# Kernel tuning notes

Measured on AMD Instinct MI355X. Metric: run time of the kernel, lower is better.

## Reference

```python
import jax, jax.numpy as jnp
import numpy as np

B, T, D, H = 4, 2048, 1024, 16
Dh = D // H          # 64 head dim
NF = Dh // 2         # 32 rotary frequencies


def setup_inputs() -> dict:
    key = jax.random.key(0)
    k0, k1, k2, k3 = jax.random.split(key, 4)
    x = jax.random.normal(k0, (B, T, D), dtype=jnp.float32)
    # 3D spatial coordinates per token, e.g. voxel positions
    coords = jax.random.uniform(k1, (B, T, 3), dtype=jnp.float32, minval=0.0, maxval=64.0)
    w_scale = 1.0 / np.sqrt(D)
    qkv_w = jax.random.normal(k2, (3 * D, D), dtype=jnp.float32) * w_scale
    qkv_b = jnp.zeros((3 * D,), dtype=jnp.float32)
    proj_w = jax.random.normal(k3, (D, D), dtype=jnp.float32) * w_scale
    proj_b = jnp.zeros((D,), dtype=jnp.float32)
    # mixed-axis rope: frequency f uses coordinate axis (f % 3), geometric period spacing within each axis group
    axes = (jnp.arange(NF) % 3).astype(jnp.int32)
    group = (jnp.arange(NF) // 3).astype(jnp.float32)
    n_per_axis = float(NF) / 3.0
    inv_freq = (10000.0 ** (-group / n_per_axis)).astype(jnp.float32)
    return {"x": x, "coords": coords, "qkv_w": qkv_w, "qkv_b": qkv_b,
            "proj_w": proj_w, "proj_b": proj_b, "inv_freq": inv_freq, "axes": axes}


def _apply_rope(t, sin, cos):
    # t: [B, H, T, Dh]; sin/cos: [B, 1, T, Dh//2]  (rotate-half convention)
    t1, t2 = jnp.split(t, 2, axis=-1)
    return jnp.concatenate([t1 * cos - t2 * sin, t1 * sin + t2 * cos], axis=-1)


def reference(x, coords, qkv_w, qkv_b, proj_w, proj_b, inv_freq, axes):
    b, t, d = x.shape
    # fused QKV projection
    qkv = (x @ qkv_w.T + qkv_b).reshape(b, t, 3, H, Dh)
    qkv = jnp.transpose(qkv, (2, 0, 3, 1, 4))     # [3, B, H, T, Dh]
    q, k, v = qkv[0], qkv[1], qkv[2]
    # vectorized per-sample rope from coords (replaces python loop over batch)
    ang = jnp.take(coords, axes, axis=-1) * inv_freq      # [B, T, NF]
    sin = jnp.sin(ang)[:, None]                            # [B, 1, T, NF]
    cos = jnp.cos(ang)[:, None]
    q = _apply_rope(q, sin, cos)
    k = _apply_rope(k, sin, cos)
    # standard scaling mode: single 1/sqrt(Dh) inside SDPA
    scale = 1.0 / np.sqrt(Dh)
    scores = jnp.einsum('bhqd,bhkd->bhqk', q, k) * scale
    attn = jax.nn.softmax(scores, axis=-1)
    out = jnp.einsum('bhqk,bhkd->bhqd', attn, v)           # [B, H, T, Dh]
    out = jnp.transpose(out, (0, 2, 1, 3)).reshape(b, t, d)
    return out @ proj_w.T + proj_b
```

## Files before the change

kernel.cpp:

```cpp
#include <hip/hip_runtime.h>
#include <hip/hip_bf16.h>

#define B_ 4
#define T_ 2048
#define D_ 1024
#define H_ 16
#define DH 64
#define NF 32
#define BH (B_*H_)
#define M_ROWS (B_*T_)

using u16 = unsigned short;
using u32 = unsigned int;

typedef __bf16 bf16x8 __attribute__((ext_vector_type(8)));
typedef float  f32x4  __attribute__((ext_vector_type(4)));

__device__ __forceinline__ u16 f2bf(float f) {
  u32 u = __float_as_uint(f);
  u32 r = u + 0x7fffu + ((u >> 16) & 1u);
  return (u16)(r >> 16);
}
__device__ __forceinline__ u16 f2bf_hw(float f) {
  __bf16 h = (__bf16)f;
  return *(u16*)&h;
}
__device__ __forceinline__ float bf2f(u16 h) {
  return __uint_as_float(((u32)h) << 16);
}

__device__ __forceinline__ void gload_lds16(const void* g, void* l) {
  __builtin_amdgcn_global_load_lds((__attribute__((address_space(1))) void*)(g),
                                   (__attribute__((address_space(3))) void*)(l),
                                   16, 0, 0);
}

__global__ __launch_bounds__(256)
void cvt_kernel(const float* __restrict__ in, u16* __restrict__ out, int n8) {
  int idx = blockIdx.x * 256 + threadIdx.x;
  if (idx >= n8) return;
  const float4* p = (const float4*)in + (long)idx * 2;
  float4 a = p[0], b = p[1];
  u32 o0 = (u32)f2bf(a.x) | ((u32)f2bf(a.y) << 16);
  u32 o1 = (u32)f2bf(a.z) | ((u32)f2bf(a.w) << 16);
  u32 o2 = (u32)f2bf(b.x) | ((u32)f2bf(b.y) << 16);
  u32 o3 = (u32)f2bf(b.z) | ((u32)f2bf(b.w) << 16);
  ((uint4*)out)[idx] = make_uint4(o0, o1, o2, o3);
}

__global__ __launch_bounds__(256)
void sincos_kernel(const float* __restrict__ coords, const float* __restrict__ inv_freq,
                   const int* __restrict__ axes, float* __restrict__ sc) {
  int idx = blockIdx.x * 256 + threadIdx.x;
  if (idx >= B_ * T_ * NF) return;
  int f = idx & 31;
  long bt = idx >> 5;
  float c = coords[bt * 3 + axes[f]];
  float ang = c * inv_freq[f];
  sc[bt * 64 + f]      = sinf(ang);
  sc[bt * 64 + 32 + f] = cosf(ang);
}

template<int OUT_F32>
__global__ __launch_bounds__(256, 2)
void gemm_bt(const u16* __restrict__ A, const u16* __restrict__ Bt,
             const float* __restrict__ bias, void* __restrict__ Cout,
             int M, int N, int K) {
  __shared__ u16 As[128 * 64];
  __shared__ u16 Bs[128 * 64];
  int nb = N >> 7;
  int bid = blockIdx.x;
  int nwg = gridDim.x;
  if ((nwg & 7) == 0) {
    int c = nwg >> 3;
    bid = (bid & 7) * c + (bid >> 3);
  }
  int bm = bid / nb, bn = bid % nb;
  long m0 = (long)bm << 7, n0 = (long)bn << 7;
  int tid = threadIdx.x;
  int lane = tid & 63, w = tid >> 6;
  int g = lane >> 4, lr = lane & 15;
  int wm = w >> 1, wn = w & 1;

  f32x4 acc[4][4] = {};

  for (int kt = 0; kt < K; kt += 64) {
    __syncthreads();
    #pragma unroll
    for (int j = 0; j < 4; ++j) {
      int ob = j * 4096 + tid * 16;
      int row = ob >> 7, col = (ob & 127) >> 1;
      u16* ldsA = As + j * 2048 + w * 512;
      u16* ldsB = Bs + j * 2048 + w * 512;
      gload_lds16(A + (m0 + row) * K + kt + col, ldsA);
      gload_lds16(Bt + (n0 + row) * K + kt + col, ldsB);
    }
    __syncthreads();
    #pragma unroll
    for (int kk = 0; kk < 2; ++kk) {
      bf16x8 af[4], bfr[4];
      #pragma unroll
      for (int i = 0; i < 4; ++i)
        af[i] = *(const bf16x8*)(As + (wm * 64 + i * 16 + lr) * 64 + kk * 32 + g * 8);
      #pragma unroll
      for (int i = 0; i < 4; ++i)
        bfr[i] = *(const bf16x8*)(Bs + (wn * 64 + i * 16 + lr) * 64 + kk * 32 + g * 8);
      #pragma unroll
      for (int mi = 0; mi < 4; ++mi)
        #pragma unroll
        for (int nj = 0; nj < 4; ++nj)
          acc[mi][nj] = __builtin_amdgcn_mfma_f32_16x16x32_bf16(af[mi], bfr[nj], acc[mi][nj], 0, 0, 0);
    }
  }
  #pragma unroll
  for (int mi = 0; mi < 4; ++mi) {
    #pragma unroll
    for (int nj = 0; nj < 4; ++nj) {
      long col = n0 + wn * 64 + nj * 16 + lr;
      float bv = bias[col];
      #pragma unroll
      for (int i = 0; i < 4; ++i) {
        long row = m0 + wm * 64 + mi * 16 + g * 4 + i;
        float v = acc[mi][nj][i] + bv;
        if (OUT_F32) ((float*)Cout)[row * (long)N + col] = v;
        else         ((u16*)Cout)[row * (long)N + col] = f2bf(v);
      }
    }
  }
}

__global__ __launch_bounds__(256)
void rope_kernel(const u16* __restrict__ qkv, const float* __restrict__ sc,
                 u16* __restrict__ qr, u16* __restrict__ kr, u16* __restrict__ vt) {
  __shared__ u16 Vsm[128 * 72];
  int bh = blockIdx.y;
  int b = bh >> 4, h = bh & 15;
  int t0 = blockIdx.x << 7;
  int tid = threadIdx.x;

  #pragma unroll
  for (int part = 0; part < 2; ++part) {
    u16* outp = part ? kr : qr;
    float qscale = part ? 1.0f : 0.125f;
    #pragma unroll
    for (int it = 0; it < 2; ++it) {
      int item = it * 256 + tid;
      int tl = item >> 2, fg = item & 3;
      long t = t0 + tl;
      long rbase = ((long)(b * T_) + t) * 3072 + part * 1024 + h * 64 + fg * 8;
      uint4 u1 = *(const uint4*)(qkv + rbase);
      uint4 u2 = *(const uint4*)(qkv + rbase + 32);
      const float* scp = sc + ((long)(b * T_) + t) * 64 + fg * 8;
      float4 sn0 = *(const float4*)(scp);
      float4 sn1 = *(const float4*)(scp + 4);
      float4 cs0 = *(const float4*)(scp + 32);
      float4 cs1 = *(const float4*)(scp + 36);
      float sn[8], cs[8], f1[8], f2[8];
      u32 w1[4] = {u1.x, u1.y, u1.z, u1.w};
      u32 w2[4] = {u2.x, u2.y, u2.z, u2.w};
      #pragma unroll
      for (int j = 0; j < 4; ++j) {
        f1[2*j]   = bf2f((u16)(w1[j] & 0xffff));
        f1[2*j+1] = bf2f((u16)(w1[j] >> 16));
        f2[2*j]   = bf2f((u16)(w2[j] & 0xffff));
        f2[2*j+1] = bf2f((u16)(w2[j] >> 16));
      }
      sn[0]=sn0.x; sn[1]=sn0.y; sn[2]=sn0.z; sn[3]=sn0.w;
      sn[4]=sn1.x; sn[5]=sn1.y; sn[6]=sn1.z; sn[7]=sn1.w;
      cs[0]=cs0.x; cs[1]=cs0.y; cs[2]=cs0.z; cs[3]=cs0.w;
      cs[4]=cs1.x; cs[5]=cs1.y; cs[6]=cs1.z; cs[7]=cs1.w;
      u32 o1[4], o2[4];
      #pragma unroll
      for (int j = 0; j < 4; ++j) {
        u16 a0 = f2bf((f1[2*j]   * cs[2*j]   - f2[2*j]   * sn[2*j])   * qscale);
        u16 a1 = f2bf((f1[2*j+1] * cs[2*j+1] - f2[2*j+1] * sn[2*j+1]) * qscale);
        u16 b0 = f2bf((f1[2*j]   * sn[2*j]   + f2[2*j]   * cs[2*j])   * qscale);
        u16 b1 = f2bf((f1[2*j+1] * sn[2*j+1] + f2[2*j+1] * cs[2*j+1]) * qscale);
        o1[j] = (u32)a0 | ((u32)a1 << 16);
        o2[j] = (u32)b0 | ((u32)b1 << 16);
      }
      long obase = ((long)bh * T_ + t) * DH + fg * 8;
      *(uint4*)(outp + obase)      = make_uint4(o1[0], o1[1], o1[2], o1[3]);
      *(uint4*)(outp + obase + 32) = make_uint4(o2[0], o2[1], o2[2], o2[3]);
    }
  }
  #pragma unroll
  for (int it = 0; it < 4; ++it) {
    int item = it * 256 + tid;
    int tl = item >> 3, dg = item & 7;
    long t = t0 + tl;
    uint4 u = *(const uint4*)(qkv + ((long)(b * T_) + t) * 3072 + 2048 + h * 64 + dg * 8);
    *(uint4*)(Vsm + tl * 72 + dg * 8) = u;
  }
  __syncthreads();
  int d = tid >> 2, tc = tid & 3;
  long obase = ((long)bh * DH + d) * T_ + t0 + tc * 32;
  #pragma unroll
  for (int c = 0; c < 4; ++c) {
    u32 o[4];
    #pragma unroll
    for (int j = 0; j < 4; ++j) {
      u16 lo = Vsm[(tc * 32 + c * 8 + 2 * j)     * 72 + d];
      u16 hi = Vsm[(tc * 32 + c * 8 + 2 * j + 1) * 72 + d];
      o[j] = (u32)lo | ((u32)hi << 16);
    }
    *(uint4*)(vt + obase + c * 8) = make_uint4(o[0], o[1], o[2], o[3]);
  }
}

__global__ __launch_bounds__(256, 3)
void attn_kernel(const u16* __restrict__ Qr, const u16* __restrict__ Kr,
                 const u16* __restrict__ Vt, u16* __restrict__ Aout) {
  __shared__ u16 Ks[2][64 * 64];
  __shared__ u16 Vs[2][64 * 64];
  __shared__ u16 Ps[4][32 * 72];
  int wg = (blockIdx.x & 7) * 128 + (blockIdx.x >> 3);
  int bh = wg >> 4;
  int b = bh >> 4, h = bh & 15;
  int q0 = (wg & 15) << 7;
  int tid = threadIdx.x;
  int lane = tid & 63, w = tid >> 6;
  int g = lane >> 4, lr = lane & 15;

  const long tbase = (long)bh * T_;
  const long vbase = (long)bh * DH;

  bf16x8 aq[2][2];
  #pragma unroll
  for (int mi = 0; mi < 2; ++mi)
    #pragma unroll
    for (int kk = 0; kk < 2; ++kk)
      aq[mi][kk] = *(const bf16x8*)(Qr + (tbase + q0 + w * 32 + mi * 16 + lr) * DH + kk * 32 + g * 8);

  f32x4 oacc[2][4] = {};
  float lsum[2][4] = {};

  const int swz0 = ((0 + g) ^ (lr & 7)) << 3;
  const int swz1 = ((4 + g) ^ (lr & 7)) << 3;

  auto STAGE = [&](int buf, int kb) {
    #pragma unroll
    for (int j = 0; j < 2; ++j) {
      int ob = j * 4096 + tid * 16;
      int row = ob >> 7;
      int c = ((ob >> 4) & 7) ^ (row & 7);
      u16* ldsK = Ks[buf] + j * 2048 + w * 512;
      u16* ldsV = Vs[buf] + j * 2048 + w * 512;
      gload_lds16(Kr + (tbase + kb + row) * DH + c * 8, ldsK);
      gload_lds16(Vt + (vbase + row) * T_ + kb + c * 8, ldsV);
    }
  };

  STAGE(0, 0);
  asm volatile("s_waitcnt vmcnt(0)" ::: "memory");
  __builtin_amdgcn_s_barrier();
  __builtin_amdgcn_sched_barrier(0);

  int cur = 0;
  for (int kt = 0; kt < T_ / 64; ++kt) {
    if (kt + 1 < T_ / 64) STAGE(cur ^ 1, (kt + 1) * 64);

    const u16* kbuf = Ks[cur];
    const u16* vbuf = Vs[cur];

    f32x4 s[2][4] = {};
    #pragma unroll
    for (int kk = 0; kk < 2; ++kk) {
      int so = kk ? swz1 : swz0;
      bf16x8 bk[4];
      #pragma unroll
      for (int nj = 0; nj < 4; ++nj)
        bk[nj] = *(const bf16x8*)(kbuf + (nj * 16 + lr) * 64 + so);
      #pragma unroll
      for (int mi = 0; mi < 2; ++mi)
        #pragma unroll
        for (int nj = 0; nj < 4; ++nj)
          s[mi][nj] = __builtin_amdgcn_mfma_f32_16x16x32_bf16(aq[mi][kk], bk[nj], s[mi][nj], 0, 0, 0);
    }

    u16* pw = Ps[w];
    #pragma unroll
    for (int mi = 0; mi < 2; ++mi) {
      #pragma unroll
      for (int i = 0; i < 4; ++i) {
        float p0 = __expf(s[mi][0][i]);
        float p1 = __expf(s[mi][1][i]);
        float p2 = __expf(s[mi][2][i]);
        float p3 = __expf(s[mi][3][i]);
        lsum[mi][i] += (p0 + p1) + (p2 + p3);
        int rb = (mi * 16 + g * 4 + i) * 72 + lr;
        pw[rb]      = f2bf_hw(p0);
        pw[rb + 16] = f2bf_hw(p1);
        pw[rb + 32] = f2bf_hw(p2);
        pw[rb + 48] = f2bf_hw(p3);
      }
    }
    asm volatile("s_waitcnt lgkmcnt(0)" ::: "memory");
    __builtin_amdgcn_sched_barrier(0);

    #pragma unroll
    for (int kk = 0; kk < 2; ++kk) {
      int so = kk ? swz1 : swz0;
      bf16x8 ap[2], bv[4];
      #pragma unroll
      for (int mi = 0; mi < 2; ++mi)
        ap[mi] = *(const bf16x8*)(pw + (mi * 16 + lr) * 72 + kk * 32 + g * 8);
      #pragma unroll
      for (int nj = 0; nj < 4; ++nj)
        bv[nj] = *(const bf16x8*)(vbuf + (nj * 16 + lr) * 64 + so);
      #pragma unroll
      for (int mi = 0; mi < 2; ++mi)
        #pragma unroll
        for (int nj = 0; nj < 4; ++nj)
          oacc[mi][nj] = __builtin_amdgcn_mfma_f32_16x16x32_bf16(ap[mi], bv[nj], oacc[mi][nj], 0, 0, 0);
    }

    __builtin_amdgcn_sched_barrier(0);
    asm volatile("s_waitcnt vmcnt(0)" ::: "memory");
    __builtin_amdgcn_s_barrier();
    __builtin_amdgcn_sched_barrier(0);
    cur ^= 1;
  }

  #pragma unroll
  for (int mi = 0; mi < 2; ++mi) {
    #pragma unroll
    for (int i = 0; i < 4; ++i) {
      float l = lsum[mi][i];
      #pragma unroll
      for (int dd = 1; dd < 16; dd <<= 1) l += __shfl_xor(l, dd);
      float inv = 1.0f / l;
      long q = q0 + w * 32 + mi * 16 + g * 4 + i;
      long obase = ((long)b * T_ + q) * D_ + h * DH;
      #pragma unroll
      for (int nj = 0; nj < 4; ++nj)
        Aout[obase + nj * 16 + lr] = f2bf_hw(oacc[mi][nj][i] * inv);
    }
  }
}

extern "C" void kernel_launch(void* const* d_in, const int* in_sizes, int n_in,
                              void* d_out, int out_size, void* d_ws, size_t ws_size,
                              hipStream_t stream) {
  const float* x        = (const float*)d_in[0];
  const float* coords   = (const float*)d_in[1];
  const float* qkv_w    = (const float*)d_in[2];
  const float* qkv_b    = (const float*)d_in[3];
  const float* proj_w   = (const float*)d_in[4];
  const float* proj_b   = (const float*)d_in[5];
  const float* inv_freq = (const float*)d_in[6];
  const int*   axes     = (const int*)d_in[7];
  float* out = (float*)d_out;

  char* ws = (char*)d_ws;
  size_t off = 0;
  auto alloc = [&](size_t bytes) -> char* {
    char* p = ws + off;
    off += (bytes + 255) & ~(size_t)255;
    return p;
  };
  u16*   xb     = (u16*)  alloc((size_t)M_ROWS * D_ * 2);
  u16*   wqkv   = (u16*)  alloc((size_t)3 * D_ * D_ * 2);
  u16*   wproj  = (u16*)  alloc((size_t)D_ * D_ * 2);
  float* sc     = (float*)alloc((size_t)M_ROWS * 64 * 4);
  u16*   qkvraw = (u16*)  alloc((size_t)M_ROWS * 3 * D_ * 2);
  u16*   qr     = (u16*)  alloc((size_t)BH * T_ * DH * 2);
  u16*   kr     = (u16*)  alloc((size_t)BH * T_ * DH * 2);
  u16*   vt     = (u16*)  alloc((size_t)BH * T_ * DH * 2);
  u16*   aout   = qkvraw;

  cvt_kernel<<<(M_ROWS * D_ / 8 + 255) / 256, 256, 0, stream>>>(x, xb, M_ROWS * D_ / 8);
  cvt_kernel<<<(3 * D_ * D_ / 8 + 255) / 256, 256, 0, stream>>>(qkv_w, wqkv, 3 * D_ * D_ / 8);
  cvt_kernel<<<(D_ * D_ / 8 + 255) / 256, 256, 0, stream>>>(proj_w, wproj, D_ * D_ / 8);
  sincos_kernel<<<(B_ * T_ * NF + 255) / 256, 256, 0, stream>>>(coords, inv_freq, axes, sc);

  gemm_bt<0><<<(M_ROWS / 128) * (3 * D_ / 128), 256, 0, stream>>>(xb, wqkv, qkv_b, qkvraw,
                                                                  M_ROWS, 3 * D_, D_);
  rope_kernel<<<dim3(T_ / 128, BH), 256, 0, stream>>>(qkvraw, sc, qr, kr, vt);
  attn_kernel<<<1024, 256, 0, stream>>>(qr, kr, vt, aout);
  gemm_bt<1><<<(M_ROWS / 128) * (D_ / 128), 256, 0, stream>>>(aout, wproj, proj_b, out,
                                                              M_ROWS, D_, D_);
}
```

Before: 232.5 us.

## Use 32x32 MFMA with transposed S to keep P in registers

The attention inner loop now computes S^T = K·Q^T using 32x32x16 bf16 MFMAs, so each lane holds scores for one query column. It then turns the exponentiated probabilities directly into the B operand for the PV MFMA via lane-xor-32 shuffles. This removes the per-warp LDS round trip for P, along with its waitcnt, and reduces the number of MFMA issues. The row sum becomes a single shuffle. The cost is extra cross-lane shuffles and higher accumulator register pressure, which could affect occupancy at launch bounds of 3.

Result: slower. 244.6 us (+5.2%).

```diff
diff --git a/kernel.cpp b/kernel.cpp
--- a/kernel.cpp
+++ b/kernel.cpp
@@ -15,6 +15,7 @@
 
 typedef __bf16 bf16x8 __attribute__((ext_vector_type(8)));
 typedef float  f32x4  __attribute__((ext_vector_type(4)));
+typedef float  f32x16 __attribute__((ext_vector_type(16)));
 
 __device__ __forceinline__ u16 f2bf(float f) {
   u32 u = __float_as_uint(f);
@@ -24,6 +25,9 @@
 __device__ __forceinline__ u16 f2bf_hw(float f) {
   __bf16 h = (__bf16)f;
   return *(u16*)&h;
+}
+__device__ __forceinline__ u32 pack2(float lo, float hi) {
+  return (u32)f2bf_hw(lo) | ((u32)f2bf_hw(hi) << 16);
 }
 __device__ __forceinline__ float bf2f(u16 h) {
   return __uint_as_float(((u32)h) << 16);
@@ -213,30 +217,26 @@
                  const u16* __restrict__ Vt, u16* __restrict__ Aout) {
   __shared__ u16 Ks[2][64 * 64];
   __shared__ u16 Vs[2][64 * 64];
-  __shared__ u16 Ps[4][32 * 72];
   int wg = (blockIdx.x & 7) * 128 + (blockIdx.x >> 3);
   int bh = wg >> 4;
   int b = bh >> 4, h = bh & 15;
   int q0 = (wg & 15) << 7;
   int tid = threadIdx.x;
   int lane = tid & 63, w = tid >> 6;
-  int g = lane >> 4, lr = lane & 15;
+  int l5 = lane & 31, hb = lane >> 5;
 
   const long tbase = (long)bh * T_;
   const long vbase = (long)bh * DH;
 
-  bf16x8 aq[2][2];
-  #pragma unroll
-  for (int mi = 0; mi < 2; ++mi)
-    #pragma unroll
-    for (int kk = 0; kk < 2; ++kk)
-      aq[mi][kk] = *(const bf16x8*)(Qr + (tbase + q0 + w * 32 + mi * 16 + lr) * DH + kk * 32 + g * 8);
-
-  f32x4 oacc[2][4] = {};
-  float lsum[2][4] = {};
-
-  const int swz0 = ((0 + g) ^ (lr & 7)) << 3;
-  const int swz1 = ((4 + g) ^ (lr & 7)) << 3;
+  bf16x8 bq[4];
+  #pragma unroll
+  for (int s = 0; s < 4; ++s)
+    bq[s] = *(const bf16x8*)(Qr + (tbase + q0 + w * 32 + l5) * DH + s * 16 + hb * 8);
+
+  f32x16 oacc0 = {}, oacc1 = {};
+  float lsum = 0.f;
+
+  const int sl = l5 & 7;
 
   auto STAGE = [&](int buf, int kb) {
     #pragma unroll
@@ -263,56 +263,51 @@
     const u16* kbuf = Ks[cur];
     const u16* vbuf = Vs[cur];
 
-    f32x4 s[2][4] = {};
-    #pragma unroll
-    for (int kk = 0; kk < 2; ++kk) {
-      int so = kk ? swz1 : swz0;
-      bf16x8 bk[4];
-      #pragma unroll
-      for (int nj = 0; nj < 4; ++nj)
-        bk[nj] = *(const bf16x8*)(kbuf + (nj * 16 + lr) * 64 + so);
-      #pragma unroll
-      for (int mi = 0; mi < 2; ++mi)
-        #pragma unroll
-        for (int nj = 0; nj < 4; ++nj)
-          s[mi][nj] = __builtin_amdgcn_mfma_f32_16x16x32_bf16(aq[mi][kk], bk[nj], s[mi][nj], 0, 0, 0);
-    }
-
-    u16* pw = Ps[w];
-    #pragma unroll
-    for (int mi = 0; mi < 2; ++mi) {
-      #pragma unroll
-      for (int i = 0; i < 4; ++i) {
-        float p0 = __expf(s[mi][0][i]);
-        float p1 = __expf(s[mi][1][i]);
-        float p2 = __expf(s[mi][2][i]);
-        float p3 = __expf(s[mi][3][i]);
-        lsum[mi][i] += (p0 + p1) + (p2 + p3);
-        int rb = (mi * 16 + g * 4 + i) * 72 + lr;
-        pw[rb]      = f2bf_hw(p0);
-        pw[rb + 16] = f2bf_hw(p1);
-        pw[rb + 32] = f2bf_hw(p2);
-        pw[rb + 48] = f2bf_hw(p3);
-      }
-    }
-    asm volatile("s_waitcnt lgkmcnt(0)" ::: "memory");
-    __builtin_amdgcn_sched_barrier(0);
-
-    #pragma unroll
-    for (int kk = 0; kk < 2; ++kk) {
-      int so = kk ? swz1 : swz0;
-      bf16x8 ap[2], bv[4];
-      #pragma unroll
-      for (int mi = 0; mi < 2; ++mi)
-        ap[mi] = *(const bf16x8*)(pw + (mi * 16 + lr) * 72 + kk * 32 + g * 8);
-      #pragma unroll
-      for (int nj = 0; nj < 4; ++nj)
-        bv[nj] = *(const bf16x8*)(vbuf + (nj * 16 + lr) * 64 + so);
-      #pragma unroll
-      for (int mi = 0; mi < 2; ++mi)
-        #pragma unroll
-        for (int nj = 0; nj < 4; ++nj)
-          oacc[mi][nj] = __builtin_amdgcn_mfma_f32_16x16x32_bf16(ap[mi], bv[nj], oacc[mi][nj], 0, 0, 0);
+    f32x16 p0 = {}, p1 = {};
+    #pragma unroll
+    for (int s = 0; s < 4; ++s) {
+      int c = ((2 * s + hb) ^ sl) * 8;
+      bf16x8 ak0 = *(const bf16x8*)(kbuf + l5 * 64 + c);
+      bf16x8 ak1 = *(const bf16x8*)(kbuf + (32 + l5) * 64 + c);
+      p0 = __builtin_amdgcn_mfma_f32_32x32x16_bf16(ak0, bq[s], p0, 0, 0, 0);
+      p1 = __builtin_amdgcn_mfma_f32_32x32x16_bf16(ak1, bq[s], p1, 0, 0, 0);
+    }
+
+    u32 pA[8], pB[8];
+    #pragma unroll
+    for (int r4 = 0; r4 < 4; ++r4) {
+      float a0 = __expf(p0[4 * r4 + 0]);
+      float a1 = __expf(p0[4 * r4 + 1]);
+      float a2 = __expf(p0[4 * r4 + 2]);
+      float a3 = __expf(p0[4 * r4 + 3]);
+      lsum += (a0 + a1) + (a2 + a3);
+      pA[r4] = pack2(a0, a1);
+      pB[r4] = pack2(a2, a3);
+      float b0 = __expf(p1[4 * r4 + 0]);
+      float b1 = __expf(p1[4 * r4 + 1]);
+      float b2 = __expf(p1[4 * r4 + 2]);
+      float b3 = __expf(p1[4 * r4 + 3]);
+      lsum += (b0 + b1) + (b2 + b3);
+      pA[4 + r4] = pack2(b0, b1);
+      pB[4 + r4] = pack2(b2, b3);
+    }
+
+    #pragma unroll
+    for (int s2 = 0; s2 < 4; ++s2) {
+      u32 xAe = (u32)__shfl_xor((int)pA[2 * s2],     32);
+      u32 xAo = (u32)__shfl_xor((int)pA[2 * s2 + 1], 32);
+      u32 xBe = (u32)__shfl_xor((int)pB[2 * s2],     32);
+      u32 xBo = (u32)__shfl_xor((int)pB[2 * s2 + 1], 32);
+      union { u32 u[4]; bf16x8 v; } bw;
+      bw.u[0] = hb ? xAo : pA[2 * s2];
+      bw.u[1] = hb ? xBo : pB[2 * s2];
+      bw.u[2] = hb ? pA[2 * s2 + 1] : xAe;
+      bw.u[3] = hb ? pB[2 * s2 + 1] : xBe;
+      int c = ((2 * s2 + hb) ^ sl) * 8;
+      bf16x8 av0 = *(const bf16x8*)(vbuf + l5 * 64 + c);
+      bf16x8 av1 = *(const bf16x8*)(vbuf + (32 + l5) * 64 + c);
+      oacc0 = __builtin_amdgcn_mfma_f32_32x32x16_bf16(av0, bw.v, oacc0, 0, 0, 0);
+      oacc1 = __builtin_amdgcn_mfma_f32_32x32x16_bf16(av1, bw.v, oacc1, 0, 0, 0);
     }
 
     __builtin_amdgcn_sched_barrier(0);
@@ -322,20 +317,18 @@
     cur ^= 1;
   }
 
-  #pragma unroll
-  for (int mi = 0; mi < 2; ++mi) {
-    #pragma unroll
-    for (int i = 0; i < 4; ++i) {
-      float l = lsum[mi][i];
-      #pragma unroll
-      for (int dd = 1; dd < 16; dd <<= 1) l += __shfl_xor(l, dd);
-      float inv = 1.0f / l;
-      long q = q0 + w * 32 + mi * 16 + g * 4 + i;
-      long obase = ((long)b * T_ + q) * D_ + h * DH;
-      #pragma unroll
-      for (int nj = 0; nj < 4; ++nj)
-        Aout[obase + nj * 16 + lr] = f2bf_hw(oacc[mi][nj][i] * inv);
-    }
+  lsum += __shfl_xor(lsum, 32);
+  float inv = 1.0f / lsum;
+  long row = (long)b * T_ + q0 + w * 32 + l5;
+  u16* ob = Aout + row * D_ + h * DH;
+  #pragma unroll
+  for (int r4 = 0; r4 < 4; ++r4) {
+    u32 w0 = pack2(oacc0[4 * r4 + 0] * inv, oacc0[4 * r4 + 1] * inv);
+    u32 w1 = pack2(oacc0[4 * r4 + 2] * inv, oacc0[4 * r4 + 3] * inv);
+    *(uint2*)(ob + r4 * 8 + hb * 4) = make_uint2(w0, w1);
+    u32 w2 = pack2(oacc1[4 * r4 + 0] * inv, oacc1[4 * r4 + 1] * inv);
+    u32 w3 = pack2(oacc1[4 * r4 + 2] * inv, oacc1[4 * r4 + 3] * inv);
+    *(uint2*)(ob + 32 + r4 * 8 + hb * 4) = make_uint2(w2, w3);
   }
 }
 
```

## Fuse RoPE and head-major scatter into QKV GEMM epilogue, use exp2 softmax

Applied to the files above, without the earlier changes.

The QKV GEMM epilogue now applies bias and rotary embedding and writes Q and K directly in [B,H,T,Dh] layout. V is written head-major to a separate buffer, and a smaller kernel then only transposes V. This removes the full bf16 qkv intermediate round trip and most of the separate rope pass. The Q scale also folds in log2(e), so the attention softmax can use exp2 instead of exp. In exchange, the epilogue stores are scattered 2-byte writes with extra sin/cos loads, which may be less efficient than the old vectorized rope stores.

Measured after the change: 244.9 us. 1.05x slower.

```diff
diff --git a/kernel.cpp b/kernel.cpp
--- a/kernel.cpp
+++ b/kernel.cpp
@@ -9,6 +9,8 @@
 #define NF 32
 #define BH (B_*H_)
 #define M_ROWS (B_*T_)
+
+#define QSCALE (0.125f * 1.44269504088896f)
 
 using u16 = unsigned short;
 using u32 = unsigned int;
@@ -61,10 +63,95 @@
   sc[bt * 64 + 32 + f] = cosf(ang);
 }
 
-template<int OUT_F32>
+__global__ __launch_bounds__(256, 2)
+void gemm_qkv(const u16* __restrict__ A, const u16* __restrict__ Bt,
+              const float* __restrict__ bias, const float* __restrict__ sc,
+              u16* __restrict__ qr, u16* __restrict__ kr, u16* __restrict__ vbuf) {
+  const int N = 3 * D_, K = D_;
+  __shared__ u16 As[128 * 64];
+  __shared__ u16 Bs[128 * 64];
+  int nb = N >> 7;
+  int bid = blockIdx.x;
+  int nwg = gridDim.x;
+  int cpx = nwg >> 3;
+  bid = (bid & 7) * cpx + (bid >> 3);
+  int bm = bid / nb, bn = bid % nb;
+  long m0 = (long)bm << 7, n0 = (long)bn << 7;
+  int tid = threadIdx.x;
+  int lane = tid & 63, w = tid >> 6;
+  int g = lane >> 4, lr = lane & 15;
+  int wm = w >> 1, wn = w & 1;
+
+  f32x4 acc[4][4] = {};
+
+  for (int kt = 0; kt < K; kt += 64) {
+    __syncthreads();
+    #pragma unroll
+    for (int j = 0; j < 4; ++j) {
+      int ob = j * 4096 + tid * 16;
+      int row = ob >> 7, col = (ob & 127) >> 1;
+      u16* ldsA = As + j * 2048 + w * 512;
+      u16* ldsB = Bs + j * 2048 + w * 512;
+      gload_lds16(A + (m0 + row) * K + kt + col, ldsA);
+      gload_lds16(Bt + (n0 + row) * K + kt + col, ldsB);
+    }
+    __syncthreads();
+    #pragma unroll
+    for (int kk = 0; kk < 2; ++kk) {
+      bf16x8 af[4], bfr[4];
+      #pragma unroll
+      for (int i = 0; i < 4; ++i)
+        af[i] = *(const bf16x8*)(As + (wm * 64 + i * 16 + lr) * 64 + kk * 32 + g * 8);
+      #pragma unroll
+      for (int i = 0; i < 4; ++i)
+        bfr[i] = *(const bf16x8*)(Bs + (wn * 64 + i * 16 + lr) * 64 + kk * 32 + g * 8);
+      #pragma unroll
+      for (int mi = 0; mi < 4; ++mi)
+        #pragma unroll
+        for (int nj = 0; nj < 4; ++nj)
+          acc[mi][nj] = __builtin_amdgcn_mfma_f32_16x16x32_bf16(af[mi], bfr[nj], acc[mi][nj], 0, 0, 0);
+    }
+  }
+
+  int part = (int)(n0 >> 10);
+  int h = ((int)(n0 & 1023) >> 6) + wn;
+  float bv[4];
+  #pragma unroll
+  for (int nj = 0; nj < 4; ++nj)
+    bv[nj] = bias[n0 + wn * 64 + nj * 16 + lr];
+
+  #pragma unroll
+  for (int mi = 0; mi < 4; ++mi) {
+    #pragma unroll
+    for (int i = 0; i < 4; ++i) {
+      long row = m0 + wm * 64 + mi * 16 + g * 4 + i;
+      int b = (int)(row >> 11), t = (int)(row & 2047);
+      long obase = ((long)(b * 16 + h) * T_ + t) * 64;
+      if (part == 2) {
+        #pragma unroll
+        for (int nj = 0; nj < 4; ++nj)
+          vbuf[obase + nj * 16 + lr] = f2bf(acc[mi][nj][i] + bv[nj]);
+      } else {
+        u16* outp = part ? kr : qr;
+        float fac = part ? 1.0f : QSCALE;
+        const float* scp = sc + row * 64;
+        #pragma unroll
+        for (int nj = 0; nj < 2; ++nj) {
+          int d = nj * 16 + lr;
+          float sn = scp[d], cs = scp[32 + d];
+          float t1 = acc[mi][nj][i]     + bv[nj];
+          float t2 = acc[mi][nj + 2][i] + bv[nj + 2];
+          outp[obase + d]      = f2bf((t1 * cs - t2 * sn) * fac);
+          outp[obase + 32 + d] = f2bf((t1 * sn + t2 * cs) * fac);
+        }
+      }
+    }
+  }
+}
+
 __global__ __launch_bounds__(256, 2)
 void gemm_bt(const u16* __restrict__ A, const u16* __restrict__ Bt,
-             const float* __restrict__ bias, void* __restrict__ Cout,
+             const float* __restrict__ bias, float* __restrict__ Cout,
              int M, int N, int K) {
   __shared__ u16 As[128 * 64];
   __shared__ u16 Bs[128 * 64];
@@ -117,79 +204,27 @@
     #pragma unroll
     for (int nj = 0; nj < 4; ++nj) {
       long col = n0 + wn * 64 + nj * 16 + lr;
-      float bv = bias[col];
+      float bvv = bias[col];
       #pragma unroll
       for (int i = 0; i < 4; ++i) {
         long row = m0 + wm * 64 + mi * 16 + g * 4 + i;
-        float v = acc[mi][nj][i] + bv;
-        if (OUT_F32) ((float*)Cout)[row * (long)N + col] = v;
-        else         ((u16*)Cout)[row * (long)N + col] = f2bf(v);
+        Cout[row * (long)N + col] = acc[mi][nj][i] + bvv;
       }
     }
   }
 }
 
 __global__ __launch_bounds__(256)
-void rope_kernel(const u16* __restrict__ qkv, const float* __restrict__ sc,
-                 u16* __restrict__ qr, u16* __restrict__ kr, u16* __restrict__ vt) {
+void vtrans_kernel(const u16* __restrict__ vbuf, u16* __restrict__ vt) {
   __shared__ u16 Vsm[128 * 72];
   int bh = blockIdx.y;
-  int b = bh >> 4, h = bh & 15;
   int t0 = blockIdx.x << 7;
   int tid = threadIdx.x;
-
-  #pragma unroll
-  for (int part = 0; part < 2; ++part) {
-    u16* outp = part ? kr : qr;
-    float qscale = part ? 1.0f : 0.125f;
-    #pragma unroll
-    for (int it = 0; it < 2; ++it) {
-      int item = it * 256 + tid;
-      int tl = item >> 2, fg = item & 3;
-      long t = t0 + tl;
-      long rbase = ((long)(b * T_) + t) * 3072 + part * 1024 + h * 64 + fg * 8;
-      uint4 u1 = *(const uint4*)(qkv + rbase);
-      uint4 u2 = *(const uint4*)(qkv + rbase + 32);
-      const float* scp = sc + ((long)(b * T_) + t) * 64 + fg * 8;
-      float4 sn0 = *(const float4*)(scp);
-      float4 sn1 = *(const float4*)(scp + 4);
-      float4 cs0 = *(const float4*)(scp + 32);
-      float4 cs1 = *(const float4*)(scp + 36);
-      float sn[8], cs[8], f1[8], f2[8];
-      u32 w1[4] = {u1.x, u1.y, u1.z, u1.w};
-      u32 w2[4] = {u2.x, u2.y, u2.z, u2.w};
-      #pragma unroll
-      for (int j = 0; j < 4; ++j) {
-        f1[2*j]   = bf2f((u16)(w1[j] & 0xffff));
-        f1[2*j+1] = bf2f((u16)(w1[j] >> 16));
-        f2[2*j]   = bf2f((u16)(w2[j] & 0xffff));
-        f2[2*j+1] = bf2f((u16)(w2[j] >> 16));
-      }
-      sn[0]=sn0.x; sn[1]=sn0.y; sn[2]=sn0.z; sn[3]=sn0.w;
-      sn[4]=sn1.x; sn[5]=sn1.y; sn[6]=sn1.z; sn[7]=sn1.w;
-      cs[0]=cs0.x; cs[1]=cs0.y; cs[2]=cs0.z; cs[3]=cs0.w;
-      cs[4]=cs1.x; cs[5]=cs1.y; cs[6]=cs1.z; cs[7]=cs1.w;
-      u32 o1[4], o2[4];
-      #pragma unroll
-      for (int j = 0; j < 4; ++j) {
-        u16 a0 = f2bf((f1[2*j]   * cs[2*j]   - f2[2*j]   * sn[2*j])   * qscale);
-        u16 a1 = f2bf((f1[2*j+1] * cs[2*j+1] - f2[2*j+1] * sn[2*j+1]) * qscale);
-        u16 b0 = f2bf((f1[2*j]   * sn[2*j]   + f2[2*j]   * cs[2*j])   * qscale);
-        u16 b1 = f2bf((f1[2*j+1] * sn[2*j+1] + f2[2*j+1] * cs[2*j+1]) * qscale);
-        o1[j] = (u32)a0 | ((u32)a1 << 16);
-        o2[j] = (u32)b0 | ((u32)b1 << 16);
-      }
-      long obase = ((long)bh * T_ + t) * DH + fg * 8;
-      *(uint4*)(outp + obase)      = make_uint4(o1[0], o1[1], o1[2], o1[3]);
-      *(uint4*)(outp + obase + 32) = make_uint4(o2[0], o2[1], o2[2], o2[3]);
-    }
-  }
   #pragma unroll
   for (int it = 0; it < 4; ++it) {
     int item = it * 256 + tid;
     int tl = item >> 3, dg = item & 7;
-    long t = t0 + tl;
-    uint4 u = *(const uint4*)(qkv + ((long)(b * T_) + t) * 3072 + 2048 + h * 64 + dg * 8);
+    uint4 u = *(const uint4*)(vbuf + ((long)bh * T_ + t0 + tl) * 64 + dg * 8);
     *(uint4*)(Vsm + tl * 72 + dg * 8) = u;
   }
   __syncthreads();
@@ -283,10 +318,10 @@
     for (int mi = 0; mi < 2; ++mi) {
       #pragma unroll
       for (int i = 0; i < 4; ++i) {
-        float p0 = __expf(s[mi][0][i]);
-        float p1 = __expf(s[mi][1][i]);
-        float p2 = __expf(s[mi][2][i]);
-        float p3 = __expf(s[mi][3][i]);
+        float p0 = __builtin_exp2f(s[mi][0][i]);
+        float p1 = __builtin_exp2f(s[mi][1][i]);
+        float p2 = __builtin_exp2f(s[mi][2][i]);
+        float p3 = __builtin_exp2f(s[mi][3][i]);
         lsum[mi][i] += (p0 + p1) + (p2 + p3);
         int rb = (mi * 16 + g * 4 + i) * 72 + lr;
         pw[rb]      = f2bf_hw(p0);
@@ -363,21 +398,21 @@
   u16*   wqkv   = (u16*)  alloc((size_t)3 * D_ * D_ * 2);
   u16*   wproj  = (u16*)  alloc((size_t)D_ * D_ * 2);
   float* sc     = (float*)alloc((size_t)M_ROWS * 64 * 4);
-  u16*   qkvraw = (u16*)  alloc((size_t)M_ROWS * 3 * D_ * 2);
   u16*   qr     = (u16*)  alloc((size_t)BH * T_ * DH * 2);
   u16*   kr     = (u16*)  alloc((size_t)BH * T_ * DH * 2);
+  u16*   vbuf   = (u16*)  alloc((size_t)BH * T_ * DH * 2);
   u16*   vt     = (u16*)  alloc((size_t)BH * T_ * DH * 2);
-  u16*   aout   = qkvraw;
+  u16*   aout   = vbuf;
 
   cvt_kernel<<<(M_ROWS * D_ / 8 + 255) / 256, 256, 0, stream>>>(x, xb, M_ROWS * D_ / 8);
   cvt_kernel<<<(3 * D_ * D_ / 8 + 255) / 256, 256, 0, stream>>>(qkv_w, wqkv, 3 * D_ * D_ / 8);
   cvt_kernel<<<(D_ * D_ / 8 + 255) / 256, 256, 0, stream>>>(proj_w, wproj, D_ * D_ / 8);
   sincos_kernel<<<(B_ * T_ * NF + 255) / 256, 256, 0, stream>>>(coords, inv_freq, axes, sc);
 
-  gemm_bt<0><<<(M_ROWS / 128) * (3 * D_ / 128), 256, 0, stream>>>(xb, wqkv, qkv_b, qkvraw,
-                                                                  M_ROWS, 3 * D_, D_);
-  rope_kernel<<<dim3(T_ / 128, BH), 256, 0, stream>>>(qkvraw, sc, qr, kr, vt);
+  gemm_qkv<<<(M_ROWS / 128) * (3 * D_ / 128), 256, 0, stream>>>(xb, wqkv, qkv_b, sc,
+                                                                qr, kr, vbuf);
+  vtrans_kernel<<<dim3(T_ / 128, BH), 256, 0, stream>>>(vbuf, vt);
   attn_kernel<<<1024, 256, 0, stream>>>(qr, kr, vt, aout);
-  gemm_bt<1><<<(M_ROWS / 128) * (D_ / 128), 256, 0, stream>>>(aout, wproj, proj_b, out,
-                                                              M_ROWS, D_, D_);
-}
+  gemm_bt<<<(M_ROWS / 128) * (D_ / 128), 256, 0, stream>>>(aout, wproj, proj_b, out,
+                                                           M_ROWS, D_, D_);
+}
```
